# Performance work log

Measured on AMD Instinct MI355X. Metric: run time of the kernel, lower is better.

Reference implementation:

```python
import jax, jax.numpy as jnp
import numpy as np

H = 256
N = 200000
B = 2048
M = 6


def _lstm_cell(x, h, c, Wih, Whh, bih, bhh):
    # PyTorch LSTM gate order: i, f, g, o
    gates = x @ Wih.T + h @ Whh.T + bih + bhh  # [B, 4H]
    i, f, g, o = jnp.split(gates, 4, axis=1)
    i = jax.nn.sigmoid(i)
    f = jax.nn.sigmoid(f)
    g = jnp.tanh(g)
    o = jax.nn.sigmoid(o)
    c_new = f * c + i * g
    h_new = o * jnp.tanh(c_new)
    return h_new, c_new


def setup_inputs() -> dict:
    key = jax.random.key(0)
    ks = jax.random.split(key, 11)
    s = 1.0 / np.sqrt(H)  # pytorch LSTM init scale
    nodes = jax.random.normal(ks[0], (N, H), jnp.float32)
    graph_id = jnp.sort(jax.random.randint(ks[1], (N,), 0, B, dtype=jnp.int64))
    return {
        "nodes": nodes,
        "graph_id": graph_id,
        "num_graphs": B,
        "Wih0": jax.random.normal(ks[2], (4 * H, 2 * H), jnp.float32) * s,
        "Whh0": jax.random.normal(ks[3], (4 * H, H), jnp.float32) * s,
        "bih0": jax.random.normal(ks[4], (4 * H,), jnp.float32) * s,
        "bhh0": jax.random.normal(ks[5], (4 * H,), jnp.float32) * s,
        "Wih1": jax.random.normal(ks[6], (4 * H, H), jnp.float32) * s,
        "Whh1": jax.random.normal(ks[7], (4 * H, H), jnp.float32) * s,
        "bih1": jax.random.normal(ks[8], (4 * H,), jnp.float32) * s,
        "bhh1": jax.random.normal(ks[9], (4 * H,), jnp.float32) * s,
    }


def reference(nodes, graph_id, num_graphs, Wih0, Whh0, bih0, bhh0, Wih1, Whh1, bih1, bhh1):
    n_hidden = nodes.shape[1]
    dt = nodes.dtype
    h0 = jnp.zeros((num_graphs, n_hidden), dt)
    c0 = jnp.zeros((num_graphs, n_hidden), dt)
    h1 = jnp.zeros((num_graphs, n_hidden), dt)
    c1 = jnp.zeros((num_graphs, n_hidden), dt)
    q = jnp.zeros((num_graphs, n_hidden), dt)
    q_star = None
    for i in range(M):
        # attention logits per node: e_v = <nodes_v, q_{g(v)}>
        e = jnp.sum(nodes * q[graph_id], axis=1)  # [N]
        # segment softmax over each graph
        emax = jax.ops.segment_max(e, graph_id, num_segments=num_graphs)
        ex = jnp.exp(e - emax[graph_id])
        denom = jax.ops.segment_sum(ex, graph_id, num_segments=num_graphs)
        a = ex / denom[graph_id]  # [N]
        # attention-weighted readout per graph
        r = jax.ops.segment_sum(a[:, None] * nodes, graph_id, num_segments=num_graphs)  # [B, H]
        q_star = jnp.concatenate([q, r], axis=1)  # [B, 2H]
        if i < M - 1:
            h0, c0 = _lstm_cell(q_star, h0, c0, Wih0, Whh0, bih0, bhh0)
            h1, c1 = _lstm_cell(h0, h1, c1, Wih1, Whh1, bih1, bhh1)
            q = h1
    return q_star
```

## Files before the change

kernel.cpp:

```cpp
#include <hip/hip_runtime.h>
#include <hip/hip_bf16.h>
#include <cstdint>

#define HDIM 256

typedef __attribute__((ext_vector_type(8))) short bf16x8;
typedef __attribute__((ext_vector_type(4))) float f32x4;

__device__ __forceinline__ float bf2f(unsigned short u) {
    union { unsigned u; float f; } v; v.u = ((unsigned)u) << 16; return v.f;
}
__device__ __forceinline__ unsigned short f2bf(float f) {
    union { float f; unsigned u; } v; v.f = f;
    unsigned u = v.u;
    return (unsigned short)((u + 0x7fffu + ((u >> 16) & 1u)) >> 16);
}
__device__ __forceinline__ void gload_lds16(const void* g, void* l) {
    __builtin_amdgcn_global_load_lds((const __attribute__((address_space(1))) void*)g,
                                     (__attribute__((address_space(3))) void*)l, 16, 0, 0);
}
__device__ __forceinline__ float fsigm(float x) {
    return 1.f / (1.f + __expf(-x));
}
__device__ __forceinline__ float ftanh(float x) {
    float ax = fabsf(x);
    float z = __expf(2.f * ax);
    float th = 1.f - 2.f / (z + 1.f);
    return copysignf(th, x);
}

__global__ void k_prep(const float* __restrict__ Wih0, const float* __restrict__ Whh0,
                       const float* __restrict__ bih0, const float* __restrict__ bhh0,
                       const float* __restrict__ Wih1, const float* __restrict__ Whh1,
                       const float* __restrict__ bih1, const float* __restrict__ bhh1,
                       unsigned short* __restrict__ W0, unsigned short* __restrict__ W1,
                       float* __restrict__ b0, float* __restrict__ b1,
                       const int* __restrict__ gid, int* __restrict__ offs, int N, int B) {
    int idx = blockIdx.x * 256 + threadIdx.x;
    const int n0 = 1024 * 768, n1 = 1024 * 512;
    if (idx < n0) {
        int r = idx / 768, k = idx - r * 768;
        int orow = ((r >> 4) & 3) * 256 + ((r >> 6) << 4) + (r & 15);
        float v = (k < 512) ? Wih0[orow * 512 + k] : Whh0[orow * 256 + (k - 512)];
        W0[idx] = f2bf(v);
    } else if (idx < n0 + n1) {
        int j = idx - n0;
        int r = j >> 9, k = j & 511;
        int orow = ((r >> 4) & 3) * 256 + ((r >> 6) << 4) + (r & 15);
        float v = (k < 256) ? Wih1[orow * 256 + k] : Whh1[orow * 256 + (k - 256)];
        W1[j] = f2bf(v);
    } else if (idx < n0 + n1 + 1024) {
        int r = idx - (n0 + n1);
        int orow = ((r >> 4) & 3) * 256 + ((r >> 6) << 4) + (r & 15);
        b0[r] = bih0[orow] + bhh0[orow];
        b1[r] = bih1[orow] + bhh1[orow];
    } else if (idx <= n0 + n1 + 1024 + B) {
        int g = idx - (n0 + n1 + 1024);
        int lo = 0, hi = N;
        while (lo < hi) { int mid = (lo + hi) >> 1; if (gid[mid] < g) lo = mid + 1; else hi = mid; }
        offs[g] = lo;
    }
}

template<bool BF>
__global__ void __launch_bounds__(256) k_mean_cast(const float* __restrict__ nodes,
                                                   const int* __restrict__ offs,
                                                   unsigned short* __restrict__ nbf,
                                                   unsigned short* __restrict__ xr, int N) {
    __shared__ float red[4 * HDIM];
    int g = blockIdx.x, t = threadIdx.x;
    int lane = t & 63, wid = t >> 6;
    int start = offs[g], end = offs[g + 1];
    int Nm1 = N - 1;
    size_t col = (size_t)lane * 4;
    float4 acc = {0.f, 0.f, 0.f, 0.f};
    for (int vi0 = start + wid * 4; vi0 < end; vi0 += 16) {
        float4 v[4];
#pragma unroll
        for (int r = 0; r < 4; ++r)
            v[r] = *(const float4*)(nodes + (size_t)min(vi0 + r, Nm1) * HDIM + col);
#pragma unroll
        for (int r = 0; r < 4; ++r) {
            if (vi0 + r < end) {
                acc.x += v[r].x; acc.y += v[r].y; acc.z += v[r].z; acc.w += v[r].w;
                if (BF) {
                    ushort4 o; o.x = f2bf(v[r].x); o.y = f2bf(v[r].y);
                    o.z = f2bf(v[r].z); o.w = f2bf(v[r].w);
                    *(ushort4*)(nbf + (size_t)(vi0 + r) * HDIM + col) = o;
                }
            }
        }
    }
    *(float4*)(red + wid * HDIM + lane * 4) = acc;
    __syncthreads();
    int n = end - start;
    float r = red[t] + red[HDIM + t] + red[2 * HDIM + t] + red[3 * HDIM + t];
    r = (n > 0) ? r / (float)n : 0.f;
    xr[(size_t)g * 768 + HDIM + t] = f2bf(r);
}

template<bool LAST>
__global__ void __launch_bounds__(256) k_attn(const unsigned short* __restrict__ nb,
                                              const int* __restrict__ offs,
                                              const float* __restrict__ q,
                                              float* __restrict__ out,
                                              unsigned short* __restrict__ xr, int N) {
    __shared__ float qs[HDIM];
    __shared__ float redr[8 * HDIM];
    __shared__ float redm[8], redd[8];
    int g = blockIdx.x, t = threadIdx.x;
    int lane = t & 63, wid = t >> 6;
    int half = lane >> 5, hl = lane & 31;
    int start = offs[g], end = offs[g + 1];
    int Nm1 = N - 1;
    float qv = q[(size_t)g * HDIM + t];
    qs[t] = qv;
    __syncthreads();
    float qv8[8];
#pragma unroll
    for (int j = 0; j < 8; ++j) qv8[j] = qs[hl * 8 + j];
    float m = -INFINITY, d = 0.f, racc[8];
#pragma unroll
    for (int j = 0; j < 8; ++j) racc[j] = 0.f;
    size_t col = (size_t)hl * 8;
    int vi0 = start + wid * 4;
    bf16x8 cura = *(const bf16x8*)(nb + (size_t)min(vi0 + half, Nm1) * HDIM + col);
    bf16x8 curb = *(const bf16x8*)(nb + (size_t)min(vi0 + 2 + half, Nm1) * HDIM + col);
    for (; vi0 < end; vi0 += 16) {
        int nvi = vi0 + 16;
        bf16x8 nxta = *(const bf16x8*)(nb + (size_t)min(nvi + half, Nm1) * HDIM + col);
        bf16x8 nxtb = *(const bf16x8*)(nb + (size_t)min(nvi + 2 + half, Nm1) * HDIM + col);
        int a = vi0 + half, b = a + 2;
        if (a < end) {
            float xa[8], xb[8];
#pragma unroll
            for (int j = 0; j < 8; ++j) {
                xa[j] = bf2f((unsigned short)cura[j]);
                xb[j] = bf2f((unsigned short)curb[j]);
            }
            float ea = 0.f, eb = 0.f;
#pragma unroll
            for (int j = 0; j < 8; ++j) {
                ea = fmaf(qv8[j], xa[j], ea);
                eb = fmaf(qv8[j], xb[j], eb);
            }
#pragma unroll
            for (int o = 16; o >= 1; o >>= 1) {
                ea += __shfl_xor(ea, o, 64);
                eb += __shfl_xor(eb, o, 64);
            }
            if (b >= end) eb = -INFINITY;
            float nm = fmaxf(fmaxf(m, ea), eb);
            float sc = __expf(m - nm);
            float wa = __expf(ea - nm);
            float wb = __expf(eb - nm);
            m = nm;
            d = fmaf(d, sc, wa + wb);
#pragma unroll
            for (int j = 0; j < 8; ++j)
                racc[j] = fmaf(racc[j], sc, fmaf(wa, xa[j], wb * xb[j]));
        }
        cura = nxta; curb = nxtb;
    }
    int g2 = wid * 2 + half;
    *(float4*)(redr + g2 * HDIM + hl * 8)     = (float4){racc[0], racc[1], racc[2], racc[3]};
    *(float4*)(redr + g2 * HDIM + hl * 8 + 4) = (float4){racc[4], racc[5], racc[6], racc[7]};
    if (hl == 0) { redm[g2] = m; redd[g2] = d; }
    __syncthreads();
    float M = -INFINITY;
#pragma unroll
    for (int i = 0; i < 8; ++i) M = fmaxf(M, redm[i]);
    float D = 0.f, R = 0.f;
#pragma unroll
    for (int i = 0; i < 8; ++i) {
        float s = (redm[i] == -INFINITY) ? 0.f : __expf(redm[i] - M);
        D += redd[i] * s;
        R += redr[i * HDIM + t] * s;
    }
    float r = (D > 0.f) ? R / D : 0.f;
    if (LAST) {
        size_t ob = (size_t)g * (2 * HDIM);
        out[ob + t] = qv;
        out[ob + HDIM + t] = r;
    } else {
        xr[(size_t)g * 768 + HDIM + t] = f2bf(r);
    }
}

template<bool LAST>
__global__ void __launch_bounds__(256) k_attn_f32(const float* __restrict__ nf,
                                                  const int* __restrict__ offs,
                                                  const float* __restrict__ q,
                                                  float* __restrict__ out,
                                                  unsigned short* __restrict__ xr) {
    __shared__ float qs[HDIM];
    __shared__ float redr[4 * HDIM];
    __shared__ float redm[4], redd[4];
    int g = blockIdx.x, t = threadIdx.x;
    int lane = t & 63, wid = t >> 6;
    int start = offs[g], end = offs[g + 1];
    float qv = q[(size_t)g * HDIM + t];
    qs[t] = qv;
    __syncthreads();
    float4 qq = *(const float4*)(qs + lane * 4);
    float m = -INFINITY, d = 0.f;
    float4 racc = {0.f, 0.f, 0.f, 0.f};
    for (int vi = start + wid; vi < end; vi += 4) {
        float4 x = *(const float4*)(nf + (size_t)vi * HDIM + lane * 4);
        float e = qq.x * x.x + qq.y * x.y + qq.z * x.z + qq.w * x.w;
#pragma unroll
        for (int o = 32; o >= 1; o >>= 1) e += __shfl_xor(e, o, 64);
        float nm = fmaxf(m, e);
        float sc = __expf(m - nm);
        float wv = __expf(e - nm);
        m = nm;
        d = d * sc + wv;
        racc.x = racc.x * sc + wv * x.x;
        racc.y = racc.y * sc + wv * x.y;
        racc.z = racc.z * sc + wv * x.z;
        racc.w = racc.w * sc + wv * x.w;
    }
    *(float4*)(redr + wid * HDIM + lane * 4) = racc;
    if (lane == 0) { redm[wid] = m; redd[wid] = d; }
    __syncthreads();
    float M = fmaxf(fmaxf(redm[0], redm[1]), fmaxf(redm[2], redm[3]));
    float D = 0.f, R = 0.f;
#pragma unroll
    for (int i = 0; i < 4; ++i) {
        float s = (redm[i] == -INFINITY) ? 0.f : __expf(redm[i] - M);
        D += redd[i] * s;
        R += redr[i * HDIM + t] * s;
    }
    float r = (D > 0.f) ? R / D : 0.f;
    if (LAST) {
        size_t ob = (size_t)g * (2 * HDIM);
        out[ob + t] = qv;
        out[ob + HDIM + t] = r;
    } else {
        xr[(size_t)g * 768 + HDIM + t] = f2bf(r);
    }
}

template<int K, int PHASE>
__global__ void __launch_bounds__(256) k_gemm_lstm(const unsigned short* __restrict__ A,
                                                   const unsigned short* __restrict__ W,
                                                   const float* __restrict__ bias_p,
                                                   float* __restrict__ c,
                                                   unsigned short* __restrict__ xa,
                                                   unsigned short* __restrict__ xb,
                                                   float* __restrict__ qout) {
    __shared__ unsigned short lA[64 * 32];
    __shared__ unsigned short lB[128 * 32];
    int t = threadIdx.x, lane = t & 63, wid = t >> 6;
    int wy = wid >> 1, wx = wid & 1;
    int brow = blockIdx.x * 64, bcol = blockIdx.y * 128;
    f32x4 acc[2][4];
#pragma unroll
    for (int i = 0; i < 2; ++i)
#pragma unroll
        for (int j = 0; j < 4; ++j) acc[i][j] = (f32x4){0.f, 0.f, 0.f, 0.f};
    int sr = t >> 2, sc = (t & 3) * 8;
    for (int k0 = 0; k0 < K; k0 += 32) {
        gload_lds16(A + (size_t)(brow + sr) * K + k0 + sc, lA + t * 8);
        gload_lds16(W + (size_t)(bcol + sr) * K + k0 + sc, lB + t * 8);
        gload_lds16(W + (size_t)(bcol + 64 + sr) * K + k0 + sc, lB + 2048 + t * 8);
        asm volatile("s_waitcnt vmcnt(0)" ::: "memory");
        __syncthreads();
        bf16x8 af[2], bfr[4];
#pragma unroll
        for (int mm = 0; mm < 2; ++mm)
            af[mm] = *(const bf16x8*)(lA + (wy * 32 + mm * 16 + (lane & 15)) * 32 + (lane >> 4) * 8);
#pragma unroll
        for (int nn = 0; nn < 4; ++nn)
            bfr[nn] = *(const bf16x8*)(lB + (wx * 64 + nn * 16 + (lane & 15)) * 32 + (lane >> 4) * 8);
#pragma unroll
        for (int mm = 0; mm < 2; ++mm)
#pragma unroll
            for (int nn = 0; nn < 4; ++nn)
                acc[mm][nn] = __builtin_amdgcn_mfma_f32_16x16x32_bf16(af[mm], bfr[nn], acc[mm][nn], 0, 0, 0);
        __syncthreads();
    }
    int f = lane & 15;
    int cg = bcol + wx * 64 + f;
    float bi = bias_p[cg], bff = bias_p[cg + 16], bg = bias_p[cg + 32], bo = bias_p[cg + 48];
    int feat = (blockIdx.y * 2 + wx) * 16 + f;
#pragma unroll
    for (int mm = 0; mm < 2; ++mm)
#pragma unroll
        for (int j = 0; j < 4; ++j) {
            int row = brow + wy * 32 + mm * 16 + (lane >> 4) * 4 + j;
            float gi = fsigm(acc[mm][0][j] + bi);
            float gf = fsigm(acc[mm][1][j] + bff);
            float gg = ftanh(acc[mm][2][j] + bg);
            float go = fsigm(acc[mm][3][j] + bo);
            size_t idx = (size_t)row * HDIM + feat;
            float cn_ = gf * c[idx] + gi * gg;
            c[idx] = cn_;
            float h = go * ftanh(cn_);
            unsigned short hb = f2bf(h);
            if (PHASE == 0) {
                xa[(size_t)row * 768 + 512 + feat] = hb;
                xb[(size_t)row * 512 + feat] = hb;
            } else {
                qout[idx] = h;
                xa[(size_t)row * 768 + feat] = hb;
                xb[(size_t)row * 512 + 256 + feat] = hb;
            }
        }
}

extern "C" void kernel_launch(void* const* d_in, const int* in_sizes, int n_in,
                              void* d_out, int out_size, void* d_ws, size_t ws_size,
                              hipStream_t stream) {
    const float* nodes = (const float*)d_in[0];
    const int* gid = (const int*)d_in[1];
    const float* Wih0 = (const float*)d_in[3];
    const float* Whh0 = (const float*)d_in[4];
    const float* bih0 = (const float*)d_in[5];
    const float* bhh0 = (const float*)d_in[6];
    const float* Wih1 = (const float*)d_in[7];
    const float* Whh1 = (const float*)d_in[8];
    const float* bih1 = (const float*)d_in[9];
    const float* bhh1 = (const float*)d_in[10];
    int N = in_sizes[0] / HDIM;
    int B = out_size / (2 * HDIM);
    float* out = (float*)d_out;

    const size_t AL = 512;
    auto rnd = [&](size_t b) { return (b + AL - 1) & ~(AL - 1); };
    size_t offs_b  = rnd((size_t)(B + 1) * 4);
    size_t q_b     = rnd((size_t)B * HDIM * 4);
    size_t xb0_b   = rnd((size_t)B * 768 * 2);
    size_t xb1_b   = rnd((size_t)B * 512 * 2);
    size_t w0_b    = rnd((size_t)1024 * 768 * 2);
    size_t w1_b    = rnd((size_t)1024 * 512 * 2);
    size_t bias_b  = rnd((size_t)1024 * 4);
    size_t nb_b    = rnd((size_t)N * HDIM * 2);
    size_t base_need = offs_b + 3 * q_b + 2 * xb0_b + 2 * xb1_b + w0_b + w1_b + 2 * bias_b;
    bool useBF = (base_need + nb_b <= ws_size);

    char* w = (char*)d_ws;
    unsigned short* nodes_bf = nullptr;
    if (useBF) { nodes_bf = (unsigned short*)w; w += nb_b; }
    int* offs = (int*)w;               w += offs_b;
    float* q  = (float*)w;             w += q_b;
    float* c0 = (float*)w;             w += q_b;
    float* c1 = (float*)w;             w += q_b;
    unsigned short* xb0v[2]; unsigned short* xb1v[2];
    xb0v[0] = (unsigned short*)w;      w += xb0_b;
    xb0v[1] = (unsigned short*)w;      w += xb0_b;
    xb1v[0] = (unsigned short*)w;      w += xb1_b;
    xb1v[1] = (unsigned short*)w;      w += xb1_b;
    unsigned short* W0 = (unsigned short*)w;  w += w0_b;
    unsigned short* W1 = (unsigned short*)w;  w += w1_b;
    float* b0 = (float*)w;             w += bias_b;
    float* b1 = (float*)w;             w += bias_b;

    hipMemsetAsync(q,  0, (size_t)B * HDIM * 4, stream);
    hipMemsetAsync(c0, 0, (size_t)B * HDIM * 4, stream);
    hipMemsetAsync(c1, 0, (size_t)B * HDIM * 4, stream);
    hipMemsetAsync(xb0v[0], 0, (size_t)B * 768 * 2, stream);
    hipMemsetAsync(xb1v[0], 0, (size_t)B * 512 * 2, stream);

    {
        int total = 1024 * 768 + 1024 * 512 + 1024 + B + 1;
        k_prep<<<dim3((total + 255) / 256), dim3(256), 0, stream>>>(
            Wih0, Whh0, bih0, bhh0, Wih1, Whh1, bih1, bhh1, W0, W1, b0, b1,
            gid, offs, N, B);
    }
    if (useBF)
        k_mean_cast<true><<<dim3(B), dim3(256), 0, stream>>>(nodes, offs, nodes_bf, xb0v[0], N);
    else
        k_mean_cast<false><<<dim3(B), dim3(256), 0, stream>>>(nodes, offs, nullptr, xb0v[0], N);

    for (int s = 0; s < 5; ++s) {
        int vr = s & 1, vw = vr ^ 1;
        k_gemm_lstm<768, 0><<<dim3(B / 64, 8), dim3(256), 0, stream>>>(
            xb0v[vr], W0, b0, c0, xb0v[vw], xb1v[vr], nullptr);
        k_gemm_lstm<512, 1><<<dim3(B / 64, 8), dim3(256), 0, stream>>>(
            xb1v[vr], W1, b1, c1, xb0v[vw], xb1v[vw], q);
        if (s < 4) {
            if (useBF)
                k_attn<false><<<dim3(B), dim3(256), 0, stream>>>(nodes_bf, offs, q, nullptr, xb0v[vw], N);
            else
                k_attn_f32<false><<<dim3(B), dim3(256), 0, stream>>>(nodes, offs, q, nullptr, xb0v[vw]);
        } else {
            if (useBF)
                k_attn<true><<<dim3(B), dim3(256), 0, stream>>>(nodes_bf, offs, q, out, nullptr, N);
            else
                k_attn_f32<true><<<dim3(B), dim3(256), 0, stream>>>(nodes, offs, q, out, nullptr);
        }
    }
}
```

Baseline: 320.1 us.

## Double-buffer GEMM LDS tiles, deepen attention prefetch, fold memsets into mean kernel

The LSTM GEMM now double-buffers its LDS tiles so the global-to-LDS load for the next K slice is issued before the MFMAs on the current one, hiding load latency at the cost of twice the shared memory. The attention kernel prefetches two iterations ahead instead of one, which adds registers. The five hipMemsetAsync calls are removed, and the needed zeroing of the x buffers and the c0 and c1 state is done inside the mean/cast kernel, saving several small launches. The q buffer is no longer zeroed, which relies on it being written before first use.

Result: slower. 327.2 us (+2.2%).

```diff
diff --git a/kernel.cpp b/kernel.cpp
--- a/kernel.cpp
+++ b/kernel.cpp
@@ -66,7 +66,10 @@
 __global__ void __launch_bounds__(256) k_mean_cast(const float* __restrict__ nodes,
                                                    const int* __restrict__ offs,
                                                    unsigned short* __restrict__ nbf,
-                                                   unsigned short* __restrict__ xr, int N) {
+                                                   unsigned short* __restrict__ xr,
+                                                   unsigned short* __restrict__ xb1z,
+                                                   float* __restrict__ c0,
+                                                   float* __restrict__ c1, int N) {
     __shared__ float red[4 * HDIM];
     int g = blockIdx.x, t = threadIdx.x;
     int lane = t & 63, wid = t >> 6;
@@ -96,7 +99,12 @@
     int n = end - start;
     float r = red[t] + red[HDIM + t] + red[2 * HDIM + t] + red[3 * HDIM + t];
     r = (n > 0) ? r / (float)n : 0.f;
+    xr[(size_t)g * 768 + t] = 0;
     xr[(size_t)g * 768 + HDIM + t] = f2bf(r);
+    xr[(size_t)g * 768 + 512 + t] = 0;
+    xb1z[(size_t)g * 512 + 256 + t] = 0;
+    c0[(size_t)g * HDIM + t] = 0.f;
+    c1[(size_t)g * HDIM + t] = 0.f;
 }
 
 template<bool LAST>
@@ -124,19 +132,20 @@
     for (int j = 0; j < 8; ++j) racc[j] = 0.f;
     size_t col = (size_t)hl * 8;
     int vi0 = start + wid * 4;
-    bf16x8 cura = *(const bf16x8*)(nb + (size_t)min(vi0 + half, Nm1) * HDIM + col);
-    bf16x8 curb = *(const bf16x8*)(nb + (size_t)min(vi0 + 2 + half, Nm1) * HDIM + col);
+    bf16x8 c0a = *(const bf16x8*)(nb + (size_t)min(vi0 + half, Nm1) * HDIM + col);
+    bf16x8 c0b = *(const bf16x8*)(nb + (size_t)min(vi0 + 2 + half, Nm1) * HDIM + col);
+    bf16x8 c1a = *(const bf16x8*)(nb + (size_t)min(vi0 + 16 + half, Nm1) * HDIM + col);
+    bf16x8 c1b = *(const bf16x8*)(nb + (size_t)min(vi0 + 18 + half, Nm1) * HDIM + col);
     for (; vi0 < end; vi0 += 16) {
-        int nvi = vi0 + 16;
-        bf16x8 nxta = *(const bf16x8*)(nb + (size_t)min(nvi + half, Nm1) * HDIM + col);
-        bf16x8 nxtb = *(const bf16x8*)(nb + (size_t)min(nvi + 2 + half, Nm1) * HDIM + col);
+        bf16x8 c2a = *(const bf16x8*)(nb + (size_t)min(vi0 + 32 + half, Nm1) * HDIM + col);
+        bf16x8 c2b = *(const bf16x8*)(nb + (size_t)min(vi0 + 34 + half, Nm1) * HDIM + col);
         int a = vi0 + half, b = a + 2;
         if (a < end) {
             float xa[8], xb[8];
 #pragma unroll
             for (int j = 0; j < 8; ++j) {
-                xa[j] = bf2f((unsigned short)cura[j]);
-                xb[j] = bf2f((unsigned short)curb[j]);
+                xa[j] = bf2f((unsigned short)c0a[j]);
+                xb[j] = bf2f((unsigned short)c0b[j]);
             }
             float ea = 0.f, eb = 0.f;
 #pragma unroll
@@ -160,7 +169,7 @@
             for (int j = 0; j < 8; ++j)
                 racc[j] = fmaf(racc[j], sc, fmaf(wa, xa[j], wb * xb[j]));
         }
-        cura = nxta; curb = nxtb;
+        c0a = c1a; c0b = c1b; c1a = c2a; c1b = c2b;
     }
     int g2 = wid * 2 + half;
     *(float4*)(redr + g2 * HDIM + hl * 8)     = (float4){racc[0], racc[1], racc[2], racc[3]};
@@ -249,8 +258,8 @@
                                                    unsigned short* __restrict__ xa,
                                                    unsigned short* __restrict__ xb,
                                                    float* __restrict__ qout) {
-    __shared__ unsigned short lA[64 * 32];
-    __shared__ unsigned short lB[128 * 32];
+    __shared__ unsigned short lA[2 * 64 * 32];
+    __shared__ unsigned short lB[2 * 128 * 32];
     int t = threadIdx.x, lane = t & 63, wid = t >> 6;
     int wy = wid >> 1, wx = wid & 1;
     int brow = blockIdx.x * 64, bcol = blockIdx.y * 128;
@@ -260,24 +269,36 @@
 #pragma unroll
         for (int j = 0; j < 4; ++j) acc[i][j] = (f32x4){0.f, 0.f, 0.f, 0.f};
     int sr = t >> 2, sc = (t & 3) * 8;
-    for (int k0 = 0; k0 < K; k0 += 32) {
-        gload_lds16(A + (size_t)(brow + sr) * K + k0 + sc, lA + t * 8);
-        gload_lds16(W + (size_t)(bcol + sr) * K + k0 + sc, lB + t * 8);
-        gload_lds16(W + (size_t)(bcol + 64 + sr) * K + k0 + sc, lB + 2048 + t * 8);
-        asm volatile("s_waitcnt vmcnt(0)" ::: "memory");
-        __syncthreads();
+    const unsigned short* gA = A + (size_t)(brow + sr) * K + sc;
+    const unsigned short* gB0 = W + (size_t)(bcol + sr) * K + sc;
+    const unsigned short* gB1 = W + (size_t)(bcol + 64 + sr) * K + sc;
+    auto stage = [&](int buf, int k0) {
+        gload_lds16(gA + k0, lA + buf * 2048 + t * 8);
+        gload_lds16(gB0 + k0, lB + buf * 4096 + t * 8);
+        gload_lds16(gB1 + k0, lB + buf * 4096 + 2048 + t * 8);
+    };
+    constexpr int NT = K / 32;
+    stage(0, 0);
+    asm volatile("s_waitcnt vmcnt(0)" ::: "memory");
+    __syncthreads();
+    for (int tt = 0; tt < NT; ++tt) {
+        int cur = tt & 1;
+        if (tt + 1 < NT) stage(cur ^ 1, (tt + 1) * 32);
+        const unsigned short* bA = lA + cur * 2048;
+        const unsigned short* bB = lB + cur * 4096;
         bf16x8 af[2], bfr[4];
 #pragma unroll
         for (int mm = 0; mm < 2; ++mm)
-            af[mm] = *(const bf16x8*)(lA + (wy * 32 + mm * 16 + (lane & 15)) * 32 + (lane >> 4) * 8);
+            af[mm] = *(const bf16x8*)(bA + (wy * 32 + mm * 16 + (lane & 15)) * 32 + (lane >> 4) * 8);
 #pragma unroll
         for (int nn = 0; nn < 4; ++nn)
-            bfr[nn] = *(const bf16x8*)(lB + (wx * 64 + nn * 16 + (lane & 15)) * 32 + (lane >> 4) * 8);
+            bfr[nn] = *(const bf16x8*)(bB + (wx * 64 + nn * 16 + (lane & 15)) * 32 + (lane >> 4) * 8);
 #pragma unroll
         for (int mm = 0; mm < 2; ++mm)
 #pragma unroll
             for (int nn = 0; nn < 4; ++nn)
                 acc[mm][nn] = __builtin_amdgcn_mfma_f32_16x16x32_bf16(af[mm], bfr[nn], acc[mm][nn], 0, 0, 0);
+        asm volatile("s_waitcnt vmcnt(0)" ::: "memory");
         __syncthreads();
     }
     int f = lane & 15;
@@ -356,12 +377,6 @@
     float* b0 = (float*)w;             w += bias_b;
     float* b1 = (float*)w;             w += bias_b;
 
-    hipMemsetAsync(q,  0, (size_t)B * HDIM * 4, stream);
-    hipMemsetAsync(c0, 0, (size_t)B * HDIM * 4, stream);
-    hipMemsetAsync(c1, 0, (size_t)B * HDIM * 4, stream);
-    hipMemsetAsync(xb0v[0], 0, (size_t)B * 768 * 2, stream);
-    hipMemsetAsync(xb1v[0], 0, (size_t)B * 512 * 2, stream);
-
     {
         int total = 1024 * 768 + 1024 * 512 + 1024 + B + 1;
         k_prep<<<dim3((total + 255) / 256), dim3(256), 0, stream>>>(
@@ -369,9 +384,11 @@
             gid, offs, N, B);
     }
     if (useBF)
-        k_mean_cast<true><<<dim3(B), dim3(256), 0, stream>>>(nodes, offs, nodes_bf, xb0v[0], N);
+        k_mean_cast<true><<<dim3(B), dim3(256), 0, stream>>>(nodes, offs, nodes_bf,
+                                                             xb0v[0], xb1v[0], c0, c1, N);
     else
-        k_mean_cast<false><<<dim3(B), dim3(256), 0, stream>>>(nodes, offs, nullptr, xb0v[0], N);
+        k_mean_cast<false><<<dim3(B), dim3(256), 0, stream>>>(nodes, offs, nullptr,
+                                                              xb0v[0], xb1v[0], c0, c1, N);
 
     for (int s = 0; s < 5; ++s) {
         int vr = s & 1, vw = vr ^ 1;
```
